# Kernel tuning notes

Measured on AMD Instinct MI355X. Metric: run time of the kernel, lower is better.

The kernel has to match this reference:

```python
import jax, jax.numpy as jnp
import numpy as np
from jax import lax

DIM = 384
NUM_HEADS = 6
STRIDE_Q = 1
STRIDE_KV = 2
BN_EPS = 1e-5
SCALE = DIM ** (-0.5)  # CvT scales by dim_out, not head_dim


def setup_inputs() -> dict:
    key = jax.random.key(0)
    ks = jax.random.split(key, 8)
    B, H, W, C = 32, 28, 28, DIM
    T = 1 + H * W
    x = jax.random.normal(ks[0], (B, T, C), dtype=jnp.float32)
    conv_w = jax.random.normal(ks[1], (3, C, 1, 3, 3), dtype=jnp.float32) * 0.1
    bn_gamma = jnp.ones((3, C), dtype=jnp.float32)
    bn_beta = jnp.zeros((3, C), dtype=jnp.float32)
    bn_mean = jnp.zeros((3, C), dtype=jnp.float32)
    bn_var = jnp.ones((3, C), dtype=jnp.float32)
    w_q = jax.random.normal(ks[2], (C, C), dtype=jnp.float32) * 0.02
    w_k = jax.random.normal(ks[3], (C, C), dtype=jnp.float32) * 0.02
    w_v = jax.random.normal(ks[4], (C, C), dtype=jnp.float32) * 0.02
    w_proj = jax.random.normal(ks[5], (C, C), dtype=jnp.float32) * 0.02
    b_proj = jnp.zeros((C,), dtype=jnp.float32)
    return {"x": x, "conv_w": conv_w, "bn_gamma": bn_gamma, "bn_beta": bn_beta,
            "bn_mean": bn_mean, "bn_var": bn_var, "w_q": w_q, "w_k": w_k,
            "w_v": w_v, "w_proj": w_proj, "b_proj": b_proj, "h": H, "w": W}


def _dw_conv_bn(x_sp, cw, gamma, beta, mean, var, stride):
    # x_sp: [B, C, H, W]; cw: [C, 1, 3, 3] depthwise (groups=C); inference BN
    C = x_sp.shape[1]
    y = lax.conv_general_dilated(
        x_sp, cw, window_strides=(stride, stride), padding=((1, 1), (1, 1)),
        feature_group_count=C, dimension_numbers=("NCHW", "OIHW", "NCHW"))
    inv = gamma * lax.rsqrt(var + BN_EPS)
    y = y * inv[None, :, None, None] + (beta - mean * inv)[None, :, None, None]
    B, Cc, Hc, Wc = y.shape
    return y.reshape(B, Cc, Hc * Wc).transpose(0, 2, 1)  # b (h w) c


def reference(x, conv_w, bn_gamma, bn_beta, bn_mean, bn_var,
              w_q, w_k, w_v, w_proj, b_proj, h, w):
    B, T, C = x.shape
    nh, hd = NUM_HEADS, C // NUM_HEADS
    cls_tok, x_tok = x[:, :1], x[:, 1:]
    x_sp = x_tok.reshape(B, h, w, C).transpose(0, 3, 1, 2)  # b c h w

    q = _dw_conv_bn(x_sp, conv_w[0], bn_gamma[0], bn_beta[0], bn_mean[0], bn_var[0], STRIDE_Q)
    k = _dw_conv_bn(x_sp, conv_w[1], bn_gamma[1], bn_beta[1], bn_mean[1], bn_var[1], STRIDE_KV)
    v = _dw_conv_bn(x_sp, conv_w[2], bn_gamma[2], bn_beta[2], bn_mean[2], bn_var[2], STRIDE_KV)

    q = jnp.concatenate([cls_tok, q], axis=1)
    k = jnp.concatenate([cls_tok, k], axis=1)
    v = jnp.concatenate([cls_tok, v], axis=1)

    def split_heads(t, wm):  # linear proj then b t (h d) -> b h t d
        t = t @ wm.T
        Bt, Tt, _ = t.shape
        return t.reshape(Bt, Tt, nh, hd).transpose(0, 2, 1, 3)

    q = split_heads(q, w_q)
    k = split_heads(k, w_k)
    v = split_heads(v, w_v)

    attn = jax.nn.softmax(jnp.einsum("bhld,bhtd->bhlt", q, k) * SCALE, axis=-1)
    out = jnp.einsum("bhlt,bhtd->bhld", attn, v)
    out = out.transpose(0, 2, 1, 3).reshape(B, -1, C)  # b t (h d)
    return out @ w_proj.T + b_proj
```

## Files before the change

### kernel.cpp

```cpp
#include <hip/hip_runtime.h>
#include <math.h>

#define B_SZ   32
#define C_DIM  384
#define H_IN   28
#define W_IN   28
#define TQ     785
#define TKV    197
#define NH     6
#define HD     64
#define SCALE_F 0.05103103630798287f
#define SCALE_L2E (0.05103103630798287f * 1.4426950408889634f)
#define BN_EPS_F 1e-5f

#define QROWS    25120
#define KVROWS   6304
#define QROWS_P  25344
#define KVROWS_P 6400
#define WELEM    147456
#define VT_LD    208

#define QT256    99
#define KVT256   25

typedef _Float16 f16;
typedef f16  f16x8 __attribute__((ext_vector_type(8)));
typedef f16  f16x4 __attribute__((ext_vector_type(4)));
typedef float f32x4 __attribute__((ext_vector_type(4)));

__device__ __forceinline__ void split16(float v, f16& h, f16& l) {
    h = (f16)v;
    l = (f16)(v - (float)h);
}

__device__ __forceinline__ void cp16(void* lds, const void* g) {
    __builtin_amdgcn_global_load_lds(
        (const __attribute__((address_space(1))) unsigned int*)g,
        (__attribute__((address_space(3))) unsigned int*)lds, 16, 0, 0);
}

__device__ __forceinline__ bool swz(int id, int yMax, int& y, int& n0) {
    int g = id / 24, w = id - g * 24;
    y = g * 8 + (w & 7);
    n0 = (w >> 3) * 128;
    return y < yMax;
}

__global__ __launch_bounds__(256) void prep_kernel(
    const float* __restrict__ wq, const float* __restrict__ wk,
    const float* __restrict__ wv, const float* __restrict__ wp,
    const float* __restrict__ conv_w,
    const float* __restrict__ gamma, const float* __restrict__ beta,
    const float* __restrict__ mean, const float* __restrict__ var,
    f16* __restrict__ Wh, f16* __restrict__ Wl,
    float* __restrict__ wAll)
{
    int idx = blockIdx.x * 256 + threadIdx.x;
    if (idx < 4 * WELEM) {
        int which = idx / WELEM, rem = idx - which * WELEM;
        const float* s = (which == 0) ? wq : (which == 1) ? wk : (which == 2) ? wv : wp;
        float v = s[rem];
        if (which == 0) v *= SCALE_L2E;
        f16 h, l;
        split16(v, h, l);
        Wh[idx] = h; Wl[idx] = l;
    } else if (idx < 4 * WELEM + 3 * C_DIM) {
        int k = idx - 4 * WELEM;
        int cv = k / C_DIM, c = k - cv * C_DIM;
        float inv = gamma[k] * rsqrtf(var[k] + BN_EPS_F);
#pragma unroll
        for (int t = 0; t < 9; ++t)
            wAll[cv * 3840 + t * C_DIM + c] = conv_w[(size_t)cv * C_DIM * 9 + c * 9 + t] * inv;
        wAll[cv * 3840 + 9 * C_DIM + c] = beta[k] - mean[k] * inv;
    }
}

__global__ __launch_bounds__(256) void fused_conv_kernel(
    const float* __restrict__ x,
    const float* __restrict__ wAll,
    f16* __restrict__ qh, f16* __restrict__ ql,
    f16* __restrict__ kh, f16* __restrict__ kl,
    f16* __restrict__ vh, f16* __restrict__ vl)
{
    __shared__ float sW[3 * 3840];
    int tid = threadIdx.x;
    int oi = blockIdx.x, b = blockIdx.y;

    if (oi == H_IN) {
        if (tid < 96) {
            int c = tid * 4;
            float4 v = *(const float4*)&x[(size_t)b * TQ * C_DIM + c];
            float a[4] = {v.x, v.y, v.z, v.w};
            f16x4 hv, lv;
#pragma unroll
            for (int u = 0; u < 4; ++u) { f16 h, l; split16(a[u], h, l); hv[u] = h; lv[u] = l; }
            size_t oq = (size_t)b * TQ * C_DIM + c;
            size_t okv = (size_t)b * TKV * C_DIM + c;
            *(f16x4*)&qh[oq] = hv;  *(f16x4*)&ql[oq] = lv;
            *(f16x4*)&kh[okv] = hv; *(f16x4*)&kl[okv] = lv;
            *(f16x4*)&vh[okv] = hv; *(f16x4*)&vl[okv] = lv;
        }
        return;
    }

#pragma unroll
    for (int i = 0; i < 12; ++i) {
        int idx = tid + 256 * i;
        if (idx < 2880) cp16(&sW[idx * 4], &wAll[idx * 4]);
    }
    __syncthreads();

    const size_t xb = (size_t)b * TQ * C_DIM + C_DIM;
    bool oi_even = (oi & 1) == 0;

    for (int it = 0; it < 11; ++it) {
        int idx = tid + 256 * it;
        if (idx >= 28 * 96) break;
        int oj = idx / 96, cg = idx - oj * 96;
        int c = cg * 4;

        float4 xv[9];
#pragma unroll
        for (int di = 0; di < 3; ++di) {
            int ii = oi + di - 1;
            bool rok = (ii >= 0) && (ii < H_IN);
#pragma unroll
            for (int dj = 0; dj < 3; ++dj) {
                int jj = oj + dj - 1;
                bool ok = rok && (jj >= 0) && (jj < W_IN);
                xv[di * 3 + dj] = ok ? *(const float4*)&x[xb + ((size_t)ii * W_IN + jj) * C_DIM + c]
                                     : make_float4(0.f, 0.f, 0.f, 0.f);
            }
        }

        {
            float4 acc = *(const float4*)&sW[0 * 3840 + 9 * C_DIM + c];
#pragma unroll
            for (int t = 0; t < 9; ++t) {
                float4 w4 = *(const float4*)&sW[0 * 3840 + t * C_DIM + c];
                acc.x += w4.x * xv[t].x; acc.y += w4.y * xv[t].y;
                acc.z += w4.z * xv[t].z; acc.w += w4.w * xv[t].w;
            }
            f16x4 hv, lv;
            float a[4] = {acc.x, acc.y, acc.z, acc.w};
#pragma unroll
            for (int u = 0; u < 4; ++u) { f16 h, l; split16(a[u], h, l); hv[u] = h; lv[u] = l; }
            size_t off = ((size_t)b * TQ + 1 + oi * W_IN + oj) * C_DIM + c;
            *(f16x4*)&qh[off] = hv;
            *(f16x4*)&ql[off] = lv;
        }

        if (oi_even && ((oj & 1) == 0)) {
            int p = (oi >> 1) * 14 + (oj >> 1);
            size_t off = ((size_t)b * TKV + 1 + p) * C_DIM + c;
#pragma unroll
            for (int cv = 1; cv <= 2; ++cv) {
                float4 acc = *(const float4*)&sW[cv * 3840 + 9 * C_DIM + c];
#pragma unroll
                for (int t = 0; t < 9; ++t) {
                    float4 w4 = *(const float4*)&sW[cv * 3840 + t * C_DIM + c];
                    acc.x += w4.x * xv[t].x; acc.y += w4.y * xv[t].y;
                    acc.z += w4.z * xv[t].z; acc.w += w4.w * xv[t].w;
                }
                f16x4 hv, lv;
                float a[4] = {acc.x, acc.y, acc.z, acc.w};
#pragma unroll
                for (int u = 0; u < 4; ++u) { f16 h, l; split16(a[u], h, l); hv[u] = h; lv[u] = l; }
                if (cv == 1) { *(f16x4*)&kh[off] = hv; *(f16x4*)&kl[off] = lv; }
                else         { *(f16x4*)&vh[off] = hv; *(f16x4*)&vl[off] = lv; }
            }
        }
    }
}

__device__ __forceinline__ void gemm_body(
    const f16* __restrict__ Ah, const f16* __restrict__ Al,
    const f16* __restrict__ Wh, const f16* __restrict__ Wl,
    const float* __restrict__ bias,
    float* __restrict__ Cf, f16* __restrict__ Coh, f16* __restrict__ Col,
    int M, int mode, int m0, int n0)
{
    __shared__ f16 lds[3 * 24576];

    const int t = threadIdx.x;
    const int wv = t >> 6, lane = t & 63;
    const int wr = (wv >> 1) * 64;
    const int wc = (wv & 1) * 64;
    const int lrow = lane & 15, quad = lane >> 4;
    const int qsw = quad ^ ((lrow >> 1) & 3);

    const int sr = t >> 2;
    const int g  = (t & 3) ^ ((t >> 3) & 3);

    const f16* gA0h = Ah + (size_t)(m0 + sr) * 384 + g * 8;
    const f16* gA1h = gA0h + 128 * 384;
    const f16* gA0l = Al + (size_t)(m0 + sr) * 384 + g * 8;
    const f16* gA1l = gA0l + 128 * 384;
    const f16* gBh  = Wh + (size_t)(n0 + sr) * 384 + g * 8;
    const f16* gBl  = Wl + (size_t)(n0 + sr) * 384 + g * 8;

#define STAGE(buf, kk) do {                                   \
        f16* d = lds + (buf) * 24576 + t * 8;                 \
        const int ko = (kk) * 32;                             \
        cp16(d,         gA0h + ko);                           \
        cp16(d + 4096,  gA1h + ko);                           \
        cp16(d + 8192,  gA0l + ko);                           \
        cp16(d + 12288, gA1l + ko);                           \
        cp16(d + 16384, gBh + ko);                            \
        cp16(d + 20480, gBl + ko);                            \
    } while (0)

    f32x4 acc[4][4];
#pragma unroll
    for (int i = 0; i < 4; ++i)
#pragma unroll
        for (int j = 0; j < 4; ++j)
            acc[i][j] = (f32x4){0.f, 0.f, 0.f, 0.f};

    STAGE(0, 0);
    STAGE(1, 1);

#pragma unroll
    for (int kk = 0; kk < 12; ++kk) {
        if (kk == 11) asm volatile("s_waitcnt vmcnt(0)" ::: "memory");
        else          asm volatile("s_waitcnt vmcnt(6)" ::: "memory");
        __builtin_amdgcn_s_barrier();
        __builtin_amdgcn_sched_barrier(0);

        if (kk < 10) {
            STAGE((kk + 2) % 3, kk + 2);
            __builtin_amdgcn_sched_barrier(0);
        }

        const f16* bp = lds + (kk % 3) * 24576;
        f16x8 ah[4], al[4], bh[4], bl[4];
#pragma unroll
        for (int i = 0; i < 4; ++i) {
            int ro = (wr + i * 16 + lrow) * 32 + qsw * 8;
            ah[i] = *(const f16x8*)&bp[ro];
            al[i] = *(const f16x8*)&bp[8192 + ro];
        }
#pragma unroll
        for (int j = 0; j < 4; ++j) {
            int ro = (wc + j * 16 + lrow) * 32 + qsw * 8;
            bh[j] = *(const f16x8*)&bp[16384 + ro];
            bl[j] = *(const f16x8*)&bp[20480 + ro];
        }
        asm volatile("s_waitcnt lgkmcnt(0)" ::: "memory");
        __builtin_amdgcn_sched_barrier(0);

        __builtin_amdgcn_s_setprio(1);
#pragma unroll
        for (int i = 0; i < 4; ++i)
#pragma unroll
            for (int j = 0; j < 4; ++j) {
                acc[i][j] = __builtin_amdgcn_mfma_f32_16x16x32_f16(ah[i], bh[j], acc[i][j], 0, 0, 0);
                acc[i][j] = __builtin_amdgcn_mfma_f32_16x16x32_f16(ah[i], bl[j], acc[i][j], 0, 0, 0);
                acc[i][j] = __builtin_amdgcn_mfma_f32_16x16x32_f16(al[i], bh[j], acc[i][j], 0, 0, 0);
            }
        __builtin_amdgcn_s_setprio(0);
    }
#undef STAGE

#pragma unroll
    for (int i = 0; i < 4; ++i) {
        int grow0 = m0 + wr + i * 16 + quad * 4;
#pragma unroll
        for (int j = 0; j < 4; ++j) {
            int gcol = n0 + wc + j * 16 + lrow;
            float bb = (bias && mode == 0) ? bias[gcol] : 0.f;
#pragma unroll
            for (int r = 0; r < 4; ++r) {
                int grow = grow0 + r;
                if (grow >= M) continue;
                float v = acc[i][j][r] + bb;
                if (mode == 0) {
                    Cf[(size_t)grow * 384 + gcol] = v;
                } else if (mode == 1) {
                    f16 h, l;
                    split16(v, h, l);
                    Coh[(size_t)grow * 384 + gcol] = h;
                    Col[(size_t)grow * 384 + gcol] = l;
                } else {
                    int bb2 = grow / TKV;
                    int key = grow - bb2 * TKV;
                    size_t off = (size_t)bb2 * 384 * VT_LD + (size_t)gcol * VT_LD + key;
                    f16 h, l;
                    split16(v, h, l);
                    Coh[off] = h;
                    Col[off] = l;
                }
            }
        }
    }
}

__global__ __launch_bounds__(512, 2) void qkv_proj_kernel(
    const f16* __restrict__ qh, const f16* __restrict__ ql,
    const f16* __restrict__ kh, const f16* __restrict__ kl,
    const f16* __restrict__ vh, const f16* __restrict__ vl,
    const f16* __restrict__ Wh, const f16* __restrict__ Wl,
    f16* __restrict__ Qph, f16* __restrict__ Qpl,
    f16* __restrict__ Kph, f16* __restrict__ Kpl,
    f16* __restrict__ VTh, f16* __restrict__ VTl,
    int yMax)
{
    int y, n0;
    if (!swz(blockIdx.x, yMax, y, n0)) return;
    if (y < QT256)
        gemm_body(qh, ql, Wh, Wl, nullptr, nullptr, Qph, Qpl, QROWS, 1, y * 256, n0);
    else if (y < QT256 + KVT256)
        gemm_body(kh, kl, Wh + WELEM, Wl + WELEM, nullptr, nullptr, Kph, Kpl,
                  KVROWS, 1, (y - QT256) * 256, n0);
    else
        gemm_body(vh, vl, Wh + 2 * WELEM, Wl + 2 * WELEM, nullptr, nullptr, VTh, VTl,
                  KVROWS, 2, (y - QT256 - KVT256) * 256, n0);
}

__global__ __launch_bounds__(512, 2) void v_proj_kernel(
    const f16* __restrict__ vh, const f16* __restrict__ vl,
    const f16* __restrict__ Wh, const f16* __restrict__ Wl,
    f16* __restrict__ VTh, f16* __restrict__ VTl)
{
    int y, n0;
    if (!swz(blockIdx.x, KVT256, y, n0)) return;
    gemm_body(vh, vl, Wh, Wl, nullptr, nullptr, VTh, VTl, KVROWS, 2, y * 256, n0);
}

__global__ __launch_bounds__(512, 2) void out_proj_kernel(
    const f16* __restrict__ Ah, const f16* __restrict__ Al,
    const f16* __restrict__ Wh, const f16* __restrict__ Wl,
    const float* __restrict__ bias, float* __restrict__ Cf)
{
    int y, n0;
    if (!swz(blockIdx.x, QT256, y, n0)) return;
    gemm_body(Ah, Al, Wh, Wl, bias, Cf, nullptr, nullptr, QROWS, 0, y * 256, n0);
}

__global__ __launch_bounds__(256) void attn_mfma4(
    const f16* __restrict__ Qh, const f16* __restrict__ Ql,
    const f16* __restrict__ Kh, const f16* __restrict__ Kl,
    const f16* __restrict__ VTh, const f16* __restrict__ VTl,
    f16* __restrict__ Oh, f16* __restrict__ Ol)
{
    __shared__ f16 sQh[2][64][32];
    __shared__ f16 sQl[2][64][32];
    __shared__ f16 sKh[2][64][32];
    __shared__ f16 sKl[2][64][32];
    __shared__ float sPs[64][68];

    int t = threadIdx.x;
    int wv = t >> 6, lane = t & 63;
    int c = lane & 15, quad = lane >> 4;
    int wq0 = wv * 16;
    int h = blockIdx.y, b = blockIdx.z;
    int q0 = blockIdx.x * 64;

    const size_t qbase  = (size_t)b * TQ * C_DIM + h * HD;
    const size_t kbase  = (size_t)b * TKV * C_DIM + h * HD;
    const size_t vtbase = (size_t)b * 384 * VT_LD + (size_t)h * HD * VT_LD;

#pragma unroll
    for (int i = 0; i < 2; ++i) {
        int idx = t + 256 * i;
        int ks = idx >> 8, row = (idx >> 2) & 63, sg = (idx & 3) * 8;
        cp16(&sQh[ks][row][sg], &Qh[qbase + (size_t)(q0 + row) * C_DIM + ks * 32 + sg]);
        cp16(&sQl[ks][row][sg], &Ql[qbase + (size_t)(q0 + row) * C_DIM + ks * 32 + sg]);
    }

    f32x4 s[4][4];
#pragma unroll
    for (int kt = 0; kt < 4; ++kt)
#pragma unroll
        for (int j = 0; j < 4; ++j)
            s[kt][j] = (f32x4){0.f, 0.f, 0.f, 0.f};

#pragma unroll
    for (int kt = 0; kt < 4; ++kt) {
        if (kt) __syncthreads();
#pragma unroll
        for (int i = 0; i < 2; ++i) {
            int idx = t + 256 * i;
            int ks = idx >> 8, row = (idx >> 2) & 63, sg = (idx & 3) * 8;
            cp16(&sKh[ks][row][sg], &Kh[kbase + (size_t)(kt * 64 + row) * C_DIM + ks * 32 + sg]);
            cp16(&sKl[ks][row][sg], &Kl[kbase + (size_t)(kt * 64 + row) * C_DIM + ks * 32 + sg]);
        }
        __syncthreads();

#pragma unroll
        for (int ks = 0; ks < 2; ++ks) {
            f16x8 qh8 = *(const f16x8*)&sQh[ks][wq0 + c][quad * 8];
            f16x8 ql8 = *(const f16x8*)&sQl[ks][wq0 + c][quad * 8];
#pragma unroll
            for (int j = 0; j < 4; ++j) {
                f16x8 kh8 = *(const f16x8*)&sKh[ks][j * 16 + c][quad * 8];
                f16x8 kl8 = *(const f16x8*)&sKl[ks][j * 16 + c][quad * 8];
                s[kt][j] = __builtin_amdgcn_mfma_f32_16x16x32_f16(qh8, kh8, s[kt][j], 0, 0, 0);
                s[kt][j] = __builtin_amdgcn_mfma_f32_16x16x32_f16(qh8, kl8, s[kt][j], 0, 0, 0);
                s[kt][j] = __builtin_amdgcn_mfma_f32_16x16x32_f16(ql8, kh8, s[kt][j], 0, 0, 0);
            }
        }
    }

    __syncthreads();

#pragma unroll
    for (int i = 0; i < 2; ++i) {
        int idx = t + 256 * i;
        int ks = idx >> 8, row = (idx >> 2) & 63, sg = (idx & 3) * 8;
        cp16(&sKh[ks][row][sg], &VTh[vtbase + (size_t)row * VT_LD + ks * 32 + sg]);
        cp16(&sKl[ks][row][sg], &VTl[vtbase + (size_t)row * VT_LD + ks * 32 + sg]);
    }

#pragma unroll
    for (int r = 0; r < 4; ++r) {
        s[3][0][r] = (c < 5) ? s[3][0][r] : -1e30f;
        s[3][1][r] = -1e30f;
        s[3][2][r] = -1e30f;
        s[3][3][r] = -1e30f;
    }

    float inv_r[4];
#pragma unroll
    for (int r = 0; r < 4; ++r) {
        float mx = -1e30f;
#pragma unroll
        for (int kt = 0; kt < 4; ++kt)
#pragma unroll
            for (int j = 0; j < 4; ++j)
                mx = fmaxf(mx, s[kt][j][r]);
        mx = fmaxf(mx, __shfl_xor(mx, 1));
        mx = fmaxf(mx, __shfl_xor(mx, 2));
        mx = fmaxf(mx, __shfl_xor(mx, 4));
        mx = fmaxf(mx, __shfl_xor(mx, 8));
        float sum = 0.f;
#pragma unroll
        for (int kt = 0; kt < 4; ++kt)
#pragma unroll
            for (int j = 0; j < 4; ++j) {
                float pv = exp2f(s[kt][j][r] - mx);
                s[kt][j][r] = pv;
                sum += pv;
            }
        sum += __shfl_xor(sum, 1);
        sum += __shfl_xor(sum, 2);
        sum += __shfl_xor(sum, 4);
        sum += __shfl_xor(sum, 8);
        inv_r[r] = 1.f / sum;
    }

    f32x4 o[4];
#pragma unroll
    for (int j = 0; j < 4; ++j) o[j] = (f32x4){0.f, 0.f, 0.f, 0.f};

#pragma unroll
    for (int vt = 0; vt < 4; ++vt) {
#pragma unroll
        for (int r = 0; r < 4; ++r)
#pragma unroll
            for (int j = 0; j < 4; ++j)
                sPs[wq0 + quad * 4 + r][j * 16 + c] = s[vt][j][r];

        __syncthreads();

#pragma unroll
        for (int ks = 0; ks < 2; ++ks) {
            float4 p0 = *(const float4*)&sPs[wq0 + c][ks * 32 + quad * 8];
            float4 p1 = *(const float4*)&sPs[wq0 + c][ks * 32 + quad * 8 + 4];
            float pf[8] = {p0.x, p0.y, p0.z, p0.w, p1.x, p1.y, p1.z, p1.w};
            f16x8 ph8, pl8;
#pragma unroll
            for (int ii = 0; ii < 8; ++ii) {
                f16 hh, ll;
                split16(pf[ii], hh, ll);
                ph8[ii] = hh; pl8[ii] = ll;
            }
#pragma unroll
            for (int j = 0; j < 4; ++j) {
                f16x8 vh8 = *(const f16x8*)&sKh[ks][j * 16 + c][quad * 8];
                f16x8 vl8 = *(const f16x8*)&sKl[ks][j * 16 + c][quad * 8];
                o[j] = __builtin_amdgcn_mfma_f32_16x16x32_f16(ph8, vh8, o[j], 0, 0, 0);
                o[j] = __builtin_amdgcn_mfma_f32_16x16x32_f16(ph8, vl8, o[j], 0, 0, 0);
                o[j] = __builtin_amdgcn_mfma_f32_16x16x32_f16(pl8, vh8, o[j], 0, 0, 0);
            }
        }

        if (vt < 3) {
            __syncthreads();
#pragma unroll
            for (int i = 0; i < 2; ++i) {
                int idx = t + 256 * i;
                int ks = idx >> 8, row = (idx >> 2) & 63, sg = (idx & 3) * 8;
                cp16(&sKh[ks][row][sg],
                     &VTh[vtbase + (size_t)row * VT_LD + (vt + 1) * 64 + ks * 32 + sg]);
                cp16(&sKl[ks][row][sg],
                     &VTl[vtbase + (size_t)row * VT_LD + (vt + 1) * 64 + ks * 32 + sg]);
            }
        }
    }

#pragma unroll
    for (int r = 0; r < 4; ++r) {
        int gq = q0 + wq0 + quad * 4 + r;
        if (gq >= TQ) continue;
        float inv = inv_r[r];
#pragma unroll
        for (int j = 0; j < 4; ++j) {
            float v = o[j][r] * inv;
            f16 hh, ll;
            split16(v, hh, ll);
            size_t off = (size_t)(b * TQ + gq) * C_DIM + h * HD + j * 16 + c;
            Oh[off] = hh;
            Ol[off] = ll;
        }
    }
}

extern "C" void kernel_launch(void* const* d_in, const int* in_sizes, int n_in,
                              void* d_out, int out_size, void* d_ws, size_t ws_size,
                              hipStream_t stream) {
    const float* x       = (const float*)d_in[0];
    const float* conv_w  = (const float*)d_in[1];
    const float* bn_g    = (const float*)d_in[2];
    const float* bn_b    = (const float*)d_in[3];
    const float* bn_m    = (const float*)d_in[4];
    const float* bn_v    = (const float*)d_in[5];
    const float* w_q     = (const float*)d_in[6];
    const float* w_k     = (const float*)d_in[7];
    const float* w_v     = (const float*)d_in[8];
    const float* w_proj  = (const float*)d_in[9];
    const float* b_proj  = (const float*)d_in[10];
    float* out = (float*)d_out;

    const size_t QSZ   = (size_t)QROWS_P * 384 * sizeof(f16);
    const size_t KVSZ  = (size_t)KVROWS_P * 384 * sizeof(f16);
    const size_t WSZ   = 4 * (size_t)WELEM * sizeof(f16);
    const size_t VTSZ  = (size_t)B_SZ * 384 * VT_LD * sizeof(f16);
    const size_t WALLS = 3 * 3840 * sizeof(float);

    char* p = (char*)d_ws;
    f16* qh  = (f16*)p; p += QSZ;
    f16* ql  = (f16*)p; p += QSZ;
    f16* vh  = (f16*)p; p += KVSZ;
    f16* vl  = (f16*)p; p += KVSZ;
    f16* kh  = (f16*)p; p += KVSZ;
    f16* kl  = (f16*)p; p += KVSZ;
    f16* Wh  = (f16*)p; p += WSZ;
    f16* Wl  = (f16*)p; p += WSZ;
    f16* Qph = (f16*)p; p += QSZ;
    f16* Qpl = (f16*)p; p += QSZ;
    f16* Kph = (f16*)p; p += KVSZ;
    f16* Kpl = (f16*)p; p += KVSZ;
    float* wAll = (float*)p; p += WALLS;

    size_t used = (size_t)(p - (char*)d_ws);
    bool sepVT = (ws_size >= used + 2 * VTSZ);
    f16 *VTh, *VTl;
    if (sepVT) {
        VTh = (f16*)p;
        VTl = VTh + (size_t)B_SZ * 384 * VT_LD;
    } else {
        VTh = kh;
        VTl = VTh + (size_t)B_SZ * 384 * VT_LD;
    }
    f16* oh = qh;
    f16* ol = ql;

    {
        int total = 4 * WELEM + 3 * C_DIM;
        prep_kernel<<<(total + 255) / 256, 256, 0, stream>>>(
            w_q, w_k, w_v, w_proj, conv_w, bn_g, bn_b, bn_m, bn_v, Wh, Wl, wAll);
    }

    {
        dim3 gc(H_IN + 1, B_SZ);
        fused_conv_kernel<<<gc, 256, 0, stream>>>(x, wAll, qh, ql, kh, kl, vh, vl);
    }

    if (sepVT) {
        int yMax = QT256 + 2 * KVT256;
        int nb = ((yMax + 7) / 8) * 24;
        qkv_proj_kernel<<<nb, 512, 0, stream>>>(qh, ql, kh, kl, vh, vl, Wh, Wl,
                                                Qph, Qpl, Kph, Kpl, VTh, VTl, yMax);
    } else {
        int yMax = QT256 + KVT256;
        int nb = ((yMax + 7) / 8) * 24;
        qkv_proj_kernel<<<nb, 512, 0, stream>>>(qh, ql, kh, kl, vh, vl, Wh, Wl,
                                                Qph, Qpl, Kph, Kpl, VTh, VTl, yMax);
        int nbv = ((KVT256 + 7) / 8) * 24;
        v_proj_kernel<<<nbv, 512, 0, stream>>>(vh, vl, Wh + 2 * WELEM, Wl + 2 * WELEM,
                                               VTh, VTl);
    }

    {
        dim3 ga((TQ + 63) / 64, NH, B_SZ);
        attn_mfma4<<<ga, 256, 0, stream>>>(Qph, Qpl, Kph, Kpl, VTh, VTl, oh, ol);
    }

    {
        int nb = ((QT256 + 7) / 8) * 24;
        out_proj_kernel<<<nb, 512, 0, stream>>>(oh, ol, Wh + 3 * WELEM, Wl + 3 * WELEM,
                                                b_proj, out);
    }
}
```

Measured before the change: 303.3 us.

## Enlarge GEMM tiles to 384x192 and restructure attention LDS pipelining

```diff
diff --git a/kernel.cpp b/kernel.cpp
--- a/kernel.cpp
+++ b/kernel.cpp
@@ -16,12 +16,12 @@
 #define QROWS    25120
 #define KVROWS   6304
 #define QROWS_P  25344
-#define KVROWS_P 6400
+#define KVROWS_P 6528
 #define WELEM    147456
 #define VT_LD    208
 
-#define QT256    99
-#define KVT256   25
+#define QT384    66
+#define KVT384   17
 
 typedef _Float16 f16;
 typedef f16  f16x8 __attribute__((ext_vector_type(8)));
@@ -40,9 +40,9 @@
 }
 
 __device__ __forceinline__ bool swz(int id, int yMax, int& y, int& n0) {
-    int g = id / 24, w = id - g * 24;
+    int g = id / 16, w = id - g * 16;
     y = g * 8 + (w & 7);
-    n0 = (w >> 3) * 128;
+    n0 = (w >> 3) * 192;
     return y < yMax;
 }
 
@@ -180,93 +180,88 @@
     float* __restrict__ Cf, f16* __restrict__ Coh, f16* __restrict__ Col,
     int M, int mode, int m0, int n0)
 {
-    __shared__ f16 lds[3 * 24576];
+    __shared__ f16 lds[2 * 36864];
 
     const int t = threadIdx.x;
     const int wv = t >> 6, lane = t & 63;
-    const int wr = (wv >> 1) * 64;
-    const int wc = (wv & 1) * 64;
+    const int wr = (wv >> 1) * 96;
+    const int wc = (wv & 1) * 96;
     const int lrow = lane & 15, quad = lane >> 4;
     const int qsw = quad ^ ((lrow >> 1) & 3);
 
-    const int sr = t >> 2;
-    const int g  = (t & 3) ^ ((t >> 3) & 3);
-
-    const f16* gA0h = Ah + (size_t)(m0 + sr) * 384 + g * 8;
-    const f16* gA1h = gA0h + 128 * 384;
-    const f16* gA0l = Al + (size_t)(m0 + sr) * 384 + g * 8;
-    const f16* gA1l = gA0l + 128 * 384;
-    const f16* gBh  = Wh + (size_t)(n0 + sr) * 384 + g * 8;
-    const f16* gBl  = Wl + (size_t)(n0 + sr) * 384 + g * 8;
+    const int sr16 = wv * 16 + (lane >> 2);
+    const int gch  = (lane & 3) ^ ((lane >> 3) & 3);
+
+    const f16* pAh = Ah + (size_t)(m0 + sr16) * 384 + gch * 8;
+    const f16* pAl = Al + (size_t)(m0 + sr16) * 384 + gch * 8;
+    const f16* pBh = Wh + (size_t)(n0 + sr16) * 384 + gch * 8;
+    const f16* pBl = Wl + (size_t)(n0 + sr16) * 384 + gch * 8;
+    const f16* p7  = (wv < 4) ? (pBh + 128 * 384) : (pBl - 64 * 384);
 
 #define STAGE(buf, kk) do {                                   \
-        f16* d = lds + (buf) * 24576 + t * 8;                 \
+        f16* db = lds + (buf) * 36864 + wv * 512 + lane * 8;  \
         const int ko = (kk) * 32;                             \
-        cp16(d,         gA0h + ko);                           \
-        cp16(d + 4096,  gA1h + ko);                           \
-        cp16(d + 8192,  gA0l + ko);                           \
-        cp16(d + 12288, gA1l + ko);                           \
-        cp16(d + 16384, gBh + ko);                            \
-        cp16(d + 20480, gBl + ko);                            \
+        cp16(db,          pAh + ko);                          \
+        cp16(db + 4096,   pAh + 128 * 384 + ko);              \
+        cp16(db + 8192,   pAh + 256 * 384 + ko);              \
+        cp16(db + 12288,  pAl + ko);                          \
+        cp16(db + 16384,  pAl + 128 * 384 + ko);              \
+        cp16(db + 20480,  pAl + 256 * 384 + ko);              \
+        cp16(db + 24576,  pBh + ko);                          \
+        cp16(db + 28672,  p7 + ko);                           \
+        cp16(db + 32768,  pBl + 64 * 384 + ko);               \
     } while (0)
 
-    f32x4 acc[4][4];
-#pragma unroll
-    for (int i = 0; i < 4; ++i)
-#pragma unroll
-        for (int j = 0; j < 4; ++j)
+    f32x4 acc[6][6];
+#pragma unroll
+    for (int i = 0; i < 6; ++i)
+#pragma unroll
+        for (int j = 0; j < 6; ++j)
             acc[i][j] = (f32x4){0.f, 0.f, 0.f, 0.f};
 
     STAGE(0, 0);
-    STAGE(1, 1);
-
-#pragma unroll
+
+#pragma unroll 2
     for (int kk = 0; kk < 12; ++kk) {
-        if (kk == 11) asm volatile("s_waitcnt vmcnt(0)" ::: "memory");
-        else          asm volatile("s_waitcnt vmcnt(6)" ::: "memory");
+        asm volatile("s_waitcnt vmcnt(0)" ::: "memory");
         __builtin_amdgcn_s_barrier();
         __builtin_amdgcn_sched_barrier(0);
-
-        if (kk < 10) {
-            STAGE((kk + 2) % 3, kk + 2);
-            __builtin_amdgcn_sched_barrier(0);
+        if (kk < 11) STAGE((kk + 1) & 1, kk + 1);
+
+        const f16* bp = lds + (kk & 1) * 36864;
+        __builtin_amdgcn_s_setprio(1);
+#pragma unroll
+        for (int jh = 0; jh < 2; ++jh) {
+            f16x8 bh[3], bl[3];
+#pragma unroll
+            for (int j3 = 0; j3 < 3; ++j3) {
+                int ro = (wc + (jh * 3 + j3) * 16 + lrow) * 32 + qsw * 8;
+                bh[j3] = *(const f16x8*)&bp[24576 + ro];
+                bl[j3] = *(const f16x8*)&bp[30720 + ro];
+            }
+#pragma unroll
+            for (int i = 0; i < 6; ++i) {
+                int ro = (wr + i * 16 + lrow) * 32 + qsw * 8;
+                f16x8 ah = *(const f16x8*)&bp[ro];
+                f16x8 al = *(const f16x8*)&bp[12288 + ro];
+#pragma unroll
+                for (int j3 = 0; j3 < 3; ++j3) {
+                    int j = jh * 3 + j3;
+                    acc[i][j] = __builtin_amdgcn_mfma_f32_16x16x32_f16(ah, bh[j3], acc[i][j], 0, 0, 0);
+                    acc[i][j] = __builtin_amdgcn_mfma_f32_16x16x32_f16(ah, bl[j3], acc[i][j], 0, 0, 0);
+                    acc[i][j] = __builtin_amdgcn_mfma_f32_16x16x32_f16(al, bh[j3], acc[i][j], 0, 0, 0);
+                }
+            }
         }
-
-        const f16* bp = lds + (kk % 3) * 24576;
-        f16x8 ah[4], al[4], bh[4], bl[4];
-#pragma unroll
-        for (int i = 0; i < 4; ++i) {
-            int ro = (wr + i * 16 + lrow) * 32 + qsw * 8;
-            ah[i] = *(const f16x8*)&bp[ro];
-            al[i] = *(const f16x8*)&bp[8192 + ro];
-        }
-#pragma unroll
-        for (int j = 0; j < 4; ++j) {
-            int ro = (wc + j * 16 + lrow) * 32 + qsw * 8;
-            bh[j] = *(const f16x8*)&bp[16384 + ro];
-            bl[j] = *(const f16x8*)&bp[20480 + ro];
-        }
-        asm volatile("s_waitcnt lgkmcnt(0)" ::: "memory");
-        __builtin_amdgcn_sched_barrier(0);
-
-        __builtin_amdgcn_s_setprio(1);
-#pragma unroll
-        for (int i = 0; i < 4; ++i)
-#pragma unroll
-            for (int j = 0; j < 4; ++j) {
-                acc[i][j] = __builtin_amdgcn_mfma_f32_16x16x32_f16(ah[i], bh[j], acc[i][j], 0, 0, 0);
-                acc[i][j] = __builtin_amdgcn_mfma_f32_16x16x32_f16(ah[i], bl[j], acc[i][j], 0, 0, 0);
-                acc[i][j] = __builtin_amdgcn_mfma_f32_16x16x32_f16(al[i], bh[j], acc[i][j], 0, 0, 0);
-            }
         __builtin_amdgcn_s_setprio(0);
     }
 #undef STAGE
 
 #pragma unroll
-    for (int i = 0; i < 4; ++i) {
+    for (int i = 0; i < 6; ++i) {
         int grow0 = m0 + wr + i * 16 + quad * 4;
 #pragma unroll
-        for (int j = 0; j < 4; ++j) {
+        for (int j = 0; j < 6; ++j) {
             int gcol = n0 + wc + j * 16 + lrow;
             float bb = (bias && mode == 0) ? bias[gcol] : 0.f;
 #pragma unroll
@@ -307,14 +302,14 @@
 {
     int y, n0;
     if (!swz(blockIdx.x, yMax, y, n0)) return;
-    if (y < QT256)
-        gemm_body(qh, ql, Wh, Wl, nullptr, nullptr, Qph, Qpl, QROWS, 1, y * 256, n0);
-    else if (y < QT256 + KVT256)
+    if (y < QT384)
+        gemm_body(qh, ql, Wh, Wl, nullptr, nullptr, Qph, Qpl, QROWS, 1, y * 384, n0);
+    else if (y < QT384 + KVT384)
         gemm_body(kh, kl, Wh + WELEM, Wl + WELEM, nullptr, nullptr, Kph, Kpl,
-                  KVROWS, 1, (y - QT256) * 256, n0);
+                  KVROWS, 1, (y - QT384) * 384, n0);
     else
         gemm_body(vh, vl, Wh + 2 * WELEM, Wl + 2 * WELEM, nullptr, nullptr, VTh, VTl,
-                  KVROWS, 2, (y - QT256 - KVT256) * 256, n0);
+                  KVROWS, 2, (y - QT384 - KVT384) * 384, n0);
 }
 
 __global__ __launch_bounds__(512, 2) void v_proj_kernel(
@@ -323,8 +318,8 @@
     f16* __restrict__ VTh, f16* __restrict__ VTl)
 {
     int y, n0;
-    if (!swz(blockIdx.x, KVT256, y, n0)) return;
-    gemm_body(vh, vl, Wh, Wl, nullptr, nullptr, VTh, VTl, KVROWS, 2, y * 256, n0);
+    if (!swz(blockIdx.x, KVT384, y, n0)) return;
+    gemm_body(vh, vl, Wh, Wl, nullptr, nullptr, VTh, VTl, KVROWS, 2, y * 384, n0);
 }
 
 __global__ __launch_bounds__(512, 2) void out_proj_kernel(
@@ -333,40 +328,61 @@
     const float* __restrict__ bias, float* __restrict__ Cf)
 {
     int y, n0;
-    if (!swz(blockIdx.x, QT256, y, n0)) return;
-    gemm_body(Ah, Al, Wh, Wl, bias, Cf, nullptr, nullptr, QROWS, 0, y * 256, n0);
-}
-
-__global__ __launch_bounds__(256) void attn_mfma4(
+    if (!swz(blockIdx.x, QT384, y, n0)) return;
+    gemm_body(Ah, Al, Wh, Wl, bias, Cf, nullptr, nullptr, QROWS, 0, y * 384, n0);
+}
+
+__global__ __launch_bounds__(256) void attn_mfma5(
     const f16* __restrict__ Qh, const f16* __restrict__ Ql,
     const f16* __restrict__ Kh, const f16* __restrict__ Kl,
     const f16* __restrict__ VTh, const f16* __restrict__ VTl,
     f16* __restrict__ Oh, f16* __restrict__ Ol)
 {
-    __shared__ f16 sQh[2][64][32];
-    __shared__ f16 sQl[2][64][32];
-    __shared__ f16 sKh[2][64][32];
-    __shared__ f16 sKl[2][64][32];
+    __shared__ f16 pool[3 * 8192];
     __shared__ float sPs[64][68];
 
-    int t = threadIdx.x;
-    int wv = t >> 6, lane = t & 63;
-    int c = lane & 15, quad = lane >> 4;
-    int wq0 = wv * 16;
-    int h = blockIdx.y, b = blockIdx.z;
-    int q0 = blockIdx.x * 64;
+    const int t = threadIdx.x;
+    const int wv = t >> 6, lane = t & 63;
+    const int c = lane & 15, quad = lane >> 4;
+    const int wq0 = wv * 16;
+    const int h = blockIdx.y, b = blockIdx.z;
+    const int q0 = blockIdx.x * 64;
+    const int qsw_a = quad ^ ((c >> 1) & 3);
+
+    const int R2 = 0, R0 = 8192, R1 = 16384;
 
     const size_t qbase  = (size_t)b * TQ * C_DIM + h * HD;
     const size_t kbase  = (size_t)b * TKV * C_DIM + h * HD;
     const size_t vtbase = (size_t)b * 384 * VT_LD + (size_t)h * HD * VT_LD;
 
-#pragma unroll
-    for (int i = 0; i < 2; ++i) {
-        int idx = t + 256 * i;
-        int ks = idx >> 8, row = (idx >> 2) & 63, sg = (idx & 3) * 8;
-        cp16(&sQh[ks][row][sg], &Qh[qbase + (size_t)(q0 + row) * C_DIM + ks * 32 + sg]);
-        cp16(&sQl[ks][row][sg], &Ql[qbase + (size_t)(q0 + row) * C_DIM + ks * 32 + sg]);
-    }
+    const int srow = wv * 16 + (lane >> 2);
+    const int gch  = (lane & 3) ^ ((lane >> 3) & 3);
+    const int ldst = wv * 512 + lane * 8;
+
+    const size_t qg = qbase + (size_t)(q0 + srow) * C_DIM + gch * 8;
+    const size_t kg = kbase + (size_t)srow * C_DIM + gch * 8;
+    const size_t vg = vtbase + (size_t)srow * VT_LD + gch * 8;
+
+#define K_ISSUE(R, KT) do {                                          \
+        size_t o_ = kg + (size_t)(KT) * 64 * C_DIM;                  \
+        cp16(pool + (R) + ldst,        &Kh[o_]);                     \
+        cp16(pool + (R) + 2048 + ldst, &Kh[o_ + 32]);                \
+        cp16(pool + (R) + 4096 + ldst, &Kl[o_]);                     \
+        cp16(pool + (R) + 6144 + ldst, &Kl[o_ + 32]);                \
+    } while (0)
+
+#define VT_ISSUE(R, VT) do {                                         \
+        size_t o_ = vg + (VT) * 64;                                  \
+        cp16(pool + (R) + ldst,        &VTh[o_]);                    \
+        cp16(pool + (R) + 2048 + ldst, &VTh[o_ + 32]);               \
+        cp16(pool + (R) + 4096 + ldst, &VTl[o_]);                    \
+        cp16(pool + (R) + 6144 + ldst, &VTl[o_ + 32]);               \
+    } while (0)
+
+#define WAIT_VM(N)  asm volatile("s_waitcnt vmcnt(" #N ")" ::: "memory")
+#define WAIT_VMLG(N) asm volatile("s_waitcnt vmcnt(" #N ") lgkmcnt(0)" ::: "memory")
+#define WAIT_LG()   asm volatile("s_waitcnt lgkmcnt(0)" ::: "memory")
+#define BAR() do { __builtin_amdgcn_s_barrier(); __builtin_amdgcn_sched_barrier(0); } while (0)
 
     f32x4 s[4][4];
 #pragma unroll
@@ -375,42 +391,55 @@
         for (int j = 0; j < 4; ++j)
             s[kt][j] = (f32x4){0.f, 0.f, 0.f, 0.f};
 
-#pragma unroll
-    for (int kt = 0; kt < 4; ++kt) {
-        if (kt) __syncthreads();
-#pragma unroll
-        for (int i = 0; i < 2; ++i) {
-            int idx = t + 256 * i;
-            int ks = idx >> 8, row = (idx >> 2) & 63, sg = (idx & 3) * 8;
-            cp16(&sKh[ks][row][sg], &Kh[kbase + (size_t)(kt * 64 + row) * C_DIM + ks * 32 + sg]);
-            cp16(&sKl[ks][row][sg], &Kl[kbase + (size_t)(kt * 64 + row) * C_DIM + ks * 32 + sg]);
-        }
-        __syncthreads();
-
-#pragma unroll
-        for (int ks = 0; ks < 2; ++ks) {
-            f16x8 qh8 = *(const f16x8*)&sQh[ks][wq0 + c][quad * 8];
-            f16x8 ql8 = *(const f16x8*)&sQl[ks][wq0 + c][quad * 8];
-#pragma unroll
-            for (int j = 0; j < 4; ++j) {
-                f16x8 kh8 = *(const f16x8*)&sKh[ks][j * 16 + c][quad * 8];
-                f16x8 kl8 = *(const f16x8*)&sKl[ks][j * 16 + c][quad * 8];
-                s[kt][j] = __builtin_amdgcn_mfma_f32_16x16x32_f16(qh8, kh8, s[kt][j], 0, 0, 0);
-                s[kt][j] = __builtin_amdgcn_mfma_f32_16x16x32_f16(qh8, kl8, s[kt][j], 0, 0, 0);
-                s[kt][j] = __builtin_amdgcn_mfma_f32_16x16x32_f16(ql8, kh8, s[kt][j], 0, 0, 0);
-            }
-        }
-    }
-
-    __syncthreads();
-
-#pragma unroll
-    for (int i = 0; i < 2; ++i) {
-        int idx = t + 256 * i;
-        int ks = idx >> 8, row = (idx >> 2) & 63, sg = (idx & 3) * 8;
-        cp16(&sKh[ks][row][sg], &VTh[vtbase + (size_t)row * VT_LD + ks * 32 + sg]);
-        cp16(&sKl[ks][row][sg], &VTl[vtbase + (size_t)row * VT_LD + ks * 32 + sg]);
-    }
+    {
+        cp16(pool + R2 + ldst,        &Qh[qg]);
+        cp16(pool + R2 + 2048 + ldst, &Qh[qg + 32]);
+        cp16(pool + R2 + 4096 + ldst, &Ql[qg]);
+        cp16(pool + R2 + 6144 + ldst, &Ql[qg + 32]);
+    }
+    K_ISSUE(R0, 0);
+    K_ISSUE(R1, 1);
+
+    f16x8 q8h[2], q8l[2];
+
+#define QK_TILE(KT, R, JMAX) do {                                              \
+        __builtin_amdgcn_s_setprio(1);                                         \
+        _Pragma("unroll") for (int ks = 0; ks < 2; ++ks) {                     \
+            _Pragma("unroll") for (int j = 0; j < (JMAX); ++j) {               \
+                int ro = (R) + ks * 2048 + (j * 16 + c) * 32 + qsw_a * 8;      \
+                f16x8 kh8 = *(const f16x8*)&pool[ro];                          \
+                f16x8 kl8 = *(const f16x8*)&pool[ro + 4096];                   \
+                s[KT][j] = __builtin_amdgcn_mfma_f32_16x16x32_f16(q8h[ks], kh8, s[KT][j], 0, 0, 0); \
+                s[KT][j] = __builtin_amdgcn_mfma_f32_16x16x32_f16(q8h[ks], kl8, s[KT][j], 0, 0, 0); \
+                s[KT][j] = __builtin_amdgcn_mfma_f32_16x16x32_f16(q8l[ks], kh8, s[KT][j], 0, 0, 0); \
+            } }                                                                \
+        __builtin_amdgcn_s_setprio(0);                                         \
+    } while (0)
+
+    WAIT_VM(4); BAR();
+#pragma unroll
+    for (int ks = 0; ks < 2; ++ks) {
+        int ro = R2 + ks * 2048 + (wq0 + c) * 32 + qsw_a * 8;
+        q8h[ks] = *(const f16x8*)&pool[ro];
+        q8l[ks] = *(const f16x8*)&pool[ro + 4096];
+    }
+    QK_TILE(0, R0, 4);
+
+    WAIT_VM(0); BAR();
+    K_ISSUE(R0, 2);
+    K_ISSUE(R2, 3);
+    QK_TILE(1, R1, 4);
+
+    WAIT_VM(4); BAR();
+    QK_TILE(2, R0, 4);
+
+    WAIT_VM(0); BAR();
+    QK_TILE(3, R2, 1);
+
+    WAIT_LG(); BAR();
+    VT_ISSUE(R0, 0);
+    VT_ISSUE(R1, 1);
+    VT_ISSUE(R2, 2);
 
 #pragma unroll
     for (int r = 0; r < 4; ++r) {
@@ -453,51 +482,51 @@
 #pragma unroll
     for (int j = 0; j < 4; ++j) o[j] = (f32x4){0.f, 0.f, 0.f, 0.f};
 
-#pragma unroll
-    for (int vt = 0; vt < 4; ++vt) {
-#pragma unroll
-        for (int r = 0; r < 4; ++r)
-#pragma unroll
-            for (int j = 0; j < 4; ++j)
-                sPs[wq0 + quad * 4 + r][j * 16 + c] = s[vt][j][r];
-
-        __syncthreads();
-
-#pragma unroll
-        for (int ks = 0; ks < 2; ++ks) {
-            float4 p0 = *(const float4*)&sPs[wq0 + c][ks * 32 + quad * 8];
-            float4 p1 = *(const float4*)&sPs[wq0 + c][ks * 32 + quad * 8 + 4];
-            float pf[8] = {p0.x, p0.y, p0.z, p0.w, p1.x, p1.y, p1.z, p1.w};
-            f16x8 ph8, pl8;
-#pragma unroll
-            for (int ii = 0; ii < 8; ++ii) {
-                f16 hh, ll;
-                split16(pf[ii], hh, ll);
-                ph8[ii] = hh; pl8[ii] = ll;
-            }
-#pragma unroll
-            for (int j = 0; j < 4; ++j) {
-                f16x8 vh8 = *(const f16x8*)&sKh[ks][j * 16 + c][quad * 8];
-                f16x8 vl8 = *(const f16x8*)&sKl[ks][j * 16 + c][quad * 8];
-                o[j] = __builtin_amdgcn_mfma_f32_16x16x32_f16(ph8, vh8, o[j], 0, 0, 0);
-                o[j] = __builtin_amdgcn_mfma_f32_16x16x32_f16(ph8, vl8, o[j], 0, 0, 0);
-                o[j] = __builtin_amdgcn_mfma_f32_16x16x32_f16(pl8, vh8, o[j], 0, 0, 0);
-            }
-        }
-
-        if (vt < 3) {
-            __syncthreads();
-#pragma unroll
-            for (int i = 0; i < 2; ++i) {
-                int idx = t + 256 * i;
-                int ks = idx >> 8, row = (idx >> 2) & 63, sg = (idx & 3) * 8;
-                cp16(&sKh[ks][row][sg],
-                     &VTh[vtbase + (size_t)row * VT_LD + (vt + 1) * 64 + ks * 32 + sg]);
-                cp16(&sKl[ks][row][sg],
-                     &VTl[vtbase + (size_t)row * VT_LD + (vt + 1) * 64 + ks * 32 + sg]);
-            }
-        }
-    }
+#define SPS_WRITE(VT) do {                                           \
+        _Pragma("unroll") for (int r = 0; r < 4; ++r)                \
+            _Pragma("unroll") for (int j = 0; j < 4; ++j)            \
+                sPs[wq0 + quad * 4 + r][j * 16 + c] = s[VT][j][r];   \
+    } while (0)
+
+#define PV_TILE(R, KSMAX) do {                                                 \
+        _Pragma("unroll") for (int ks = 0; ks < (KSMAX); ++ks) {               \
+            float4 p0 = *(const float4*)&sPs[wq0 + c][ks * 32 + quad * 8];     \
+            float4 p1 = *(const float4*)&sPs[wq0 + c][ks * 32 + quad * 8 + 4]; \
+            float pf[8] = {p0.x, p0.y, p0.z, p0.w, p1.x, p1.y, p1.z, p1.w};    \
+            f16x8 ph8, pl8;                                                    \
+            _Pragma("unroll") for (int ii = 0; ii < 8; ++ii) {                 \
+                f16 hh, ll; split16(pf[ii], hh, ll); ph8[ii] = hh; pl8[ii] = ll; } \
+            __builtin_amdgcn_s_setprio(1);                                     \
+            _Pragma("unroll") for (int j = 0; j < 4; ++j) {                    \
+                int ro = (R) + ks * 2048 + (j * 16 + c) * 32 + qsw_a * 8;      \
+                f16x8 vh8 = *(const f16x8*)&pool[ro];                          \
+                f16x8 vl8 = *(const f16x8*)&pool[ro + 4096];                   \
+                o[j] = __builtin_amdgcn_mfma_f32_16x16x32_f16(ph8, vh8, o[j], 0, 0, 0); \
+                o[j] = __builtin_amdgcn_mfma_f32_16x16x32_f16(ph8, vl8, o[j], 0, 0, 0); \
+                o[j] = __builtin_amdgcn_mfma_f32_16x16x32_f16(pl8, vh8, o[j], 0, 0, 0); \
+            }                                                                  \
+            __builtin_amdgcn_s_setprio(0);                                     \
+        } } while (0)
+
+    SPS_WRITE(0);
+    WAIT_VMLG(8); BAR();
+    PV_TILE(R0, 2);
+
+    WAIT_LG(); BAR();
+    VT_ISSUE(R0, 3);
+    SPS_WRITE(1);
+    WAIT_VMLG(8); BAR();
+    PV_TILE(R1, 2);
+
+    WAIT_LG(); BAR();
+    SPS_WRITE(2);
+    WAIT_VMLG(4); BAR();
+    PV_TILE(R2, 2);
+
+    WAIT_LG(); BAR();
+    SPS_WRITE(3);
+    WAIT_VMLG(0); BAR();
+    PV_TILE(R0, 1);
 
 #pragma unroll
     for (int r = 0; r < 4; ++r) {
@@ -514,6 +543,15 @@
             Ol[off] = ll;
         }
     }
+#undef K_ISSUE
+#undef VT_ISSUE
+#undef QK_TILE
+#undef PV_TILE
+#undef SPS_WRITE
+#undef WAIT_VM
+#undef WAIT_VMLG
+#undef WAIT_LG
+#undef BAR
 }
 
 extern "C" void kernel_launch(void* const* d_in, const int* in_sizes, int n_in,
@@ -578,27 +616,27 @@
     }
 
     if (sepVT) {
-        int yMax = QT256 + 2 * KVT256;
-        int nb = ((yMax + 7) / 8) * 24;
+        int yMax = QT384 + 2 * KVT384;
+        int nb = ((yMax + 7) / 8) * 16;
         qkv_proj_kernel<<<nb, 512, 0, stream>>>(qh, ql, kh, kl, vh, vl, Wh, Wl,
                                                 Qph, Qpl, Kph, Kpl, VTh, VTl, yMax);
     } else {
-        int yMax = QT256 + KVT256;
-        int nb = ((yMax + 7) / 8) * 24;
+        int yMax = QT384 + KVT384;
+        int nb = ((yMax + 7) / 8) * 16;
         qkv_proj_kernel<<<nb, 512, 0, stream>>>(qh, ql, kh, kl, vh, vl, Wh, Wl,
                                                 Qph, Qpl, Kph, Kpl, VTh, VTl, yMax);
-        int nbv = ((KVT256 + 7) / 8) * 24;
+        int nbv = ((KVT384 + 7) / 8) * 16;
         v_proj_kernel<<<nbv, 512, 0, stream>>>(vh, vl, Wh + 2 * WELEM, Wl + 2 * WELEM,
                                                VTh, VTl);
     }
 
     {
         dim3 ga((TQ + 63) / 64, NH, B_SZ);
-        attn_mfma4<<<ga, 256, 0, stream>>>(Qph, Qpl, Kph, Kpl, VTh, VTl, oh, ol);
+        attn_mfma5<<<ga, 256, 0, stream>>>(Qph, Qpl, Kph, Kpl, VTh, VTl, oh, ol);
     }
 
     {
-        int nb = ((QT256 + 7) / 8) * 24;
+        int nb = ((QT384 + 7) / 8) * 16;
         out_proj_kernel<<<nb, 512, 0, stream>>>(oh, ol, Wh + 3 * WELEM, Wl + 3 * WELEM,
                                                 b_proj, out);
     }
```

Result: slower. 342.3 us (+12.9%).

## Retile projection GEMMs to 128x384 blocks with double buffering

Applied to the files above, without the earlier changes.

```diff
diff --git a/kernel.cpp b/kernel.cpp
--- a/kernel.cpp
+++ b/kernel.cpp
@@ -1,5 +1,6 @@
 #include <hip/hip_runtime.h>
 #include <math.h>
+
 
 #define B_SZ   32
 #define C_DIM  384
@@ -16,12 +17,12 @@
 #define QROWS    25120
 #define KVROWS   6304
 #define QROWS_P  25344
-#define KVROWS_P 6400
+#define KVROWS_P 6528
 #define WELEM    147456
 #define VT_LD    208
 
-#define QT256    99
-#define KVT256   25
+#define QT128    198
+#define KVT128   51
 
 typedef _Float16 f16;
 typedef f16  f16x8 __attribute__((ext_vector_type(8)));
@@ -37,13 +38,6 @@
     __builtin_amdgcn_global_load_lds(
         (const __attribute__((address_space(1))) unsigned int*)g,
         (__attribute__((address_space(3))) unsigned int*)lds, 16, 0, 0);
-}
-
-__device__ __forceinline__ bool swz(int id, int yMax, int& y, int& n0) {
-    int g = id / 24, w = id - g * 24;
-    y = g * 8 + (w & 7);
-    n0 = (w >> 3) * 128;
-    return y < yMax;
 }
 
 __global__ __launch_bounds__(256) void prep_kernel(
@@ -178,73 +172,68 @@
     const f16* __restrict__ Wh, const f16* __restrict__ Wl,
     const float* __restrict__ bias,
     float* __restrict__ Cf, f16* __restrict__ Coh, f16* __restrict__ Col,
-    int M, int mode, int m0, int n0)
-{
-    __shared__ f16 lds[3 * 24576];
+    int M, int mode, int m0)
+{
+    __shared__ f16 lds[2][32768];
 
     const int t = threadIdx.x;
     const int wv = t >> 6, lane = t & 63;
-    const int wr = (wv >> 1) * 64;
-    const int wc = (wv & 1) * 64;
+    const int wr = (wv >> 2) * 64;
+    const int wc = (wv & 3) * 96;
     const int lrow = lane & 15, quad = lane >> 4;
     const int qsw = quad ^ ((lrow >> 1) & 3);
 
-    const int sr = t >> 2;
-    const int g  = (t & 3) ^ ((t >> 3) & 3);
-
-    const f16* gA0h = Ah + (size_t)(m0 + sr) * 384 + g * 8;
-    const f16* gA1h = gA0h + 128 * 384;
-    const f16* gA0l = Al + (size_t)(m0 + sr) * 384 + g * 8;
-    const f16* gA1l = gA0l + 128 * 384;
-    const f16* gBh  = Wh + (size_t)(n0 + sr) * 384 + g * 8;
-    const f16* gBl  = Wl + (size_t)(n0 + sr) * 384 + g * 8;
+    const int r0 = t >> 2;
+    const int g0 = (t & 3) ^ ((t >> 3) & 3);
+
+    const f16* pAh = Ah + (size_t)(m0 + r0) * 384 + g0 * 8;
+    const f16* pAl = Al + (size_t)(m0 + r0) * 384 + g0 * 8;
+    const f16* pBh = Wh + (size_t)r0 * 384 + g0 * 8;
+    const f16* pBl = Wl + (size_t)r0 * 384 + g0 * 8;
 
 #define STAGE(buf, kk) do {                                   \
-        f16* d = lds + (buf) * 24576 + t * 8;                 \
+        f16* d = &lds[buf][t * 8];                            \
         const int ko = (kk) * 32;                             \
-        cp16(d,         gA0h + ko);                           \
-        cp16(d + 4096,  gA1h + ko);                           \
-        cp16(d + 8192,  gA0l + ko);                           \
-        cp16(d + 12288, gA1l + ko);                           \
-        cp16(d + 16384, gBh + ko);                            \
-        cp16(d + 20480, gBl + ko);                            \
+        cp16(d,         pAh + ko);                            \
+        cp16(d + 4096,  pAl + ko);                            \
+        cp16(d + 8192,  pBh + ko);                            \
+        cp16(d + 12288, pBh + 128 * 384 + ko);                \
+        cp16(d + 16384, pBh + 256 * 384 + ko);                \
+        cp16(d + 20480, pBl + ko);                            \
+        cp16(d + 24576, pBl + 128 * 384 + ko);                \
+        cp16(d + 28672, pBl + 256 * 384 + ko);                \
     } while (0)
 
-    f32x4 acc[4][4];
+    f32x4 acc[4][6];
 #pragma unroll
     for (int i = 0; i < 4; ++i)
 #pragma unroll
-        for (int j = 0; j < 4; ++j)
+        for (int j = 0; j < 6; ++j)
             acc[i][j] = (f32x4){0.f, 0.f, 0.f, 0.f};
 
     STAGE(0, 0);
-    STAGE(1, 1);
-
-#pragma unroll
+
+#pragma unroll 2
     for (int kk = 0; kk < 12; ++kk) {
-        if (kk == 11) asm volatile("s_waitcnt vmcnt(0)" ::: "memory");
-        else          asm volatile("s_waitcnt vmcnt(6)" ::: "memory");
+        asm volatile("s_waitcnt vmcnt(0)" ::: "memory");
         __builtin_amdgcn_s_barrier();
         __builtin_amdgcn_sched_barrier(0);
-
-        if (kk < 10) {
-            STAGE((kk + 2) % 3, kk + 2);
-            __builtin_amdgcn_sched_barrier(0);
-        }
-
-        const f16* bp = lds + (kk % 3) * 24576;
-        f16x8 ah[4], al[4], bh[4], bl[4];
+        if (kk < 11) STAGE((kk + 1) & 1, kk + 1);
+        __builtin_amdgcn_sched_barrier(0);
+
+        const f16* bp = lds[kk & 1];
+        f16x8 ah[4], al[4], bh[6], bl[6];
 #pragma unroll
         for (int i = 0; i < 4; ++i) {
             int ro = (wr + i * 16 + lrow) * 32 + qsw * 8;
             ah[i] = *(const f16x8*)&bp[ro];
-            al[i] = *(const f16x8*)&bp[8192 + ro];
-        }
-#pragma unroll
-        for (int j = 0; j < 4; ++j) {
-            int ro = (wc + j * 16 + lrow) * 32 + qsw * 8;
-            bh[j] = *(const f16x8*)&bp[16384 + ro];
-            bl[j] = *(const f16x8*)&bp[20480 + ro];
+            al[i] = *(const f16x8*)&bp[4096 + ro];
+        }
+#pragma unroll
+        for (int j = 0; j < 6; ++j) {
+            int ro = 8192 + (wc + j * 16 + lrow) * 32 + qsw * 8;
+            bh[j] = *(const f16x8*)&bp[ro];
+            bl[j] = *(const f16x8*)&bp[12288 + ro];
         }
         asm volatile("s_waitcnt lgkmcnt(0)" ::: "memory");
         __builtin_amdgcn_sched_barrier(0);
@@ -253,7 +242,7 @@
 #pragma unroll
         for (int i = 0; i < 4; ++i)
 #pragma unroll
-            for (int j = 0; j < 4; ++j) {
+            for (int j = 0; j < 6; ++j) {
                 acc[i][j] = __builtin_amdgcn_mfma_f32_16x16x32_f16(ah[i], bh[j], acc[i][j], 0, 0, 0);
                 acc[i][j] = __builtin_amdgcn_mfma_f32_16x16x32_f16(ah[i], bl[j], acc[i][j], 0, 0, 0);
                 acc[i][j] = __builtin_amdgcn_mfma_f32_16x16x32_f16(al[i], bh[j], acc[i][j], 0, 0, 0);
@@ -266,8 +255,8 @@
     for (int i = 0; i < 4; ++i) {
         int grow0 = m0 + wr + i * 16 + quad * 4;
 #pragma unroll
-        for (int j = 0; j < 4; ++j) {
-            int gcol = n0 + wc + j * 16 + lrow;
+        for (int j = 0; j < 6; ++j) {
+            int gcol = wc + j * 16 + lrow;
             float bb = (bias && mode == 0) ? bias[gcol] : 0.f;
 #pragma unroll
             for (int r = 0; r < 4; ++r) {
@@ -305,16 +294,16 @@
     f16* __restrict__ VTh, f16* __restrict__ VTl,
     int yMax)
 {
-    int y, n0;
-    if (!swz(blockIdx.x, yMax, y, n0)) return;
-    if (y < QT256)
-        gemm_body(qh, ql, Wh, Wl, nullptr, nullptr, Qph, Qpl, QROWS, 1, y * 256, n0);
-    else if (y < QT256 + KVT256)
+    int y = blockIdx.x;
+    if (y >= yMax) return;
+    if (y < QT128)
+        gemm_body(qh, ql, Wh, Wl, nullptr, nullptr, Qph, Qpl, QROWS, 1, y * 128);
+    else if (y < QT128 + KVT128)
         gemm_body(kh, kl, Wh + WELEM, Wl + WELEM, nullptr, nullptr, Kph, Kpl,
-                  KVROWS, 1, (y - QT256) * 256, n0);
+                  KVROWS, 1, (y - QT128) * 128);
     else
         gemm_body(vh, vl, Wh + 2 * WELEM, Wl + 2 * WELEM, nullptr, nullptr, VTh, VTl,
-                  KVROWS, 2, (y - QT256 - KVT256) * 256, n0);
+                  KVROWS, 2, (y - QT128 - KVT128) * 128);
 }
 
 __global__ __launch_bounds__(512, 2) void v_proj_kernel(
@@ -322,9 +311,9 @@
     const f16* __restrict__ Wh, const f16* __restrict__ Wl,
     f16* __restrict__ VTh, f16* __restrict__ VTl)
 {
-    int y, n0;
-    if (!swz(blockIdx.x, KVT256, y, n0)) return;
-    gemm_body(vh, vl, Wh, Wl, nullptr, nullptr, VTh, VTl, KVROWS, 2, y * 256, n0);
+    int y = blockIdx.x;
+    if (y >= KVT128) return;
+    gemm_body(vh, vl, Wh, Wl, nullptr, nullptr, VTh, VTl, KVROWS, 2, y * 128);
 }
 
 __global__ __launch_bounds__(512, 2) void out_proj_kernel(
@@ -332,9 +321,9 @@
     const f16* __restrict__ Wh, const f16* __restrict__ Wl,
     const float* __restrict__ bias, float* __restrict__ Cf)
 {
-    int y, n0;
-    if (!swz(blockIdx.x, QT256, y, n0)) return;
-    gemm_body(Ah, Al, Wh, Wl, bias, Cf, nullptr, nullptr, QROWS, 0, y * 256, n0);
+    int y = blockIdx.x;
+    if (y >= QT128) return;
+    gemm_body(Ah, Al, Wh, Wl, bias, Cf, nullptr, nullptr, QROWS, 0, y * 128);
 }
 
 __global__ __launch_bounds__(256) void attn_mfma4(
@@ -578,18 +567,15 @@
     }
 
     if (sepVT) {
-        int yMax = QT256 + 2 * KVT256;
-        int nb = ((yMax + 7) / 8) * 24;
-        qkv_proj_kernel<<<nb, 512, 0, stream>>>(qh, ql, kh, kl, vh, vl, Wh, Wl,
-                                                Qph, Qpl, Kph, Kpl, VTh, VTl, yMax);
+        int yMax = QT128 + 2 * KVT128;
+        qkv_proj_kernel<<<yMax, 512, 0, stream>>>(qh, ql, kh, kl, vh, vl, Wh, Wl,
+                                                  Qph, Qpl, Kph, Kpl, VTh, VTl, yMax);
     } else {
-        int yMax = QT256 + KVT256;
-        int nb = ((yMax + 7) / 8) * 24;
-        qkv_proj_kernel<<<nb, 512, 0, stream>>>(qh, ql, kh, kl, vh, vl, Wh, Wl,
-                                                Qph, Qpl, Kph, Kpl, VTh, VTl, yMax);
-        int nbv = ((KVT256 + 7) / 8) * 24;
-        v_proj_kernel<<<nbv, 512, 0, stream>>>(vh, vl, Wh + 2 * WELEM, Wl + 2 * WELEM,
-                                               VTh, VTl);
+        int yMax = QT128 + KVT128;
+        qkv_proj_kernel<<<yMax, 512, 0, stream>>>(qh, ql, kh, kl, vh, vl, Wh, Wl,
+                                                  Qph, Qpl, Kph, Kpl, VTh, VTl, yMax);
+        v_proj_kernel<<<KVT128, 512, 0, stream>>>(vh, vl, Wh + 2 * WELEM, Wl + 2 * WELEM,
+                                                  VTh, VTl);
     }
 
     {
@@ -598,8 +584,7 @@
     }
 
     {
-        int nb = ((QT256 + 7) / 8) * 24;
-        out_proj_kernel<<<nb, 512, 0, stream>>>(oh, ol, Wh + 3 * WELEM, Wl + 3 * WELEM,
-                                                b_proj, out);
-    }
-}
+        out_proj_kernel<<<QT128, 512, 0, stream>>>(oh, ol, Wh + 3 * WELEM, Wl + 3 * WELEM,
+                                                   b_proj, out);
+    }
+}
```

Result: slower. 320.9 us (+5.8%).
